# Kernel optimization log

Measured on AMD Instinct MI355X. Metric: run time of the kernel, lower is better.

Reference implementation:

```python
import jax, jax.numpy as jnp
import numpy as np

N, E, B = 50000, 600000, 64
ANN, D, STEPS, ETYPES, CLS = 64, 128, 5, 4, 10


def setup_inputs() -> dict:
    key = jax.random.key(0)
    ks = jax.random.split(key, 12)
    return {
        "annotation": jax.random.normal(ks[0], (N, ANN), jnp.float32),
        "src": jax.random.randint(ks[1], (E,), 0, N),
        "dst": jax.random.randint(ks[2], (E,), 0, N),
        "etypes": jax.random.randint(ks[3], (E,), 0, ETYPES),
        "node2graph": jnp.sort(jax.random.randint(ks[4], (N,), 0, B)),
        "labels": jax.random.randint(ks[5], (B,), 0, CLS),
        "W_lin": jax.random.normal(ks[6], (ETYPES, D, D), jnp.float32) / np.sqrt(D),
        "b_lin": jnp.zeros((ETYPES, D), jnp.float32),
        "W_ih": jax.random.normal(ks[7], (3 * D, D), jnp.float32) / np.sqrt(D),
        "W_hh": jax.random.normal(ks[8], (3 * D, D), jnp.float32) / np.sqrt(D),
        "b_ih": jnp.zeros((3 * D,), jnp.float32),
        "b_hh": jnp.zeros((3 * D,), jnp.float32),
        "gate_w": jax.random.normal(ks[9], (1, ANN + D), jnp.float32) / np.sqrt(ANN + D),
        "gate_b": jnp.zeros((1,), jnp.float32),
        "out_w": jax.random.normal(ks[10], (CLS, ANN + D), jnp.float32) / np.sqrt(ANN + D),
        "out_b": jnp.zeros((CLS,), jnp.float32),
    }


def reference(annotation, src, dst, etypes, node2graph, labels,
              W_lin, b_lin, W_ih, W_hh, b_ih, b_hh,
              gate_w, gate_b, out_w, out_b):
    n = annotation.shape[0]
    d = W_lin.shape[-1]
    nb = labels.shape[0]
    # h1 = [annotation | zeros]  -> [N, D]
    h = jnp.concatenate(
        [annotation, jnp.zeros((n, d - annotation.shape[1]), annotation.dtype)], -1)

    def step(hc, _):
        # per-edge-type linear transform of all nodes: [K, N, D]
        all_t = jnp.einsum('nd,kod->kno', hc, W_lin) + b_lin[:, None, :]
        m = all_t[etypes, src]                                  # [E, D] messages
        a = jax.ops.segment_sum(m, dst, num_segments=n)         # [N, D] aggregate
        # torch GRUCell: gates ordered (reset, update, new)
        gi = a @ W_ih.T + b_ih
        gh = hc @ W_hh.T + b_hh
        i_r, i_z, i_n = jnp.split(gi, 3, axis=-1)
        h_r, h_z, h_n = jnp.split(gh, 3, axis=-1)
        r = jax.nn.sigmoid(i_r + h_r)
        z = jax.nn.sigmoid(i_z + h_z)
        nt = jnp.tanh(i_n + r * h_n)
        return (1.0 - z) * nt + z * hc, None

    h, _ = jax.lax.scan(step, h, None, length=STEPS)
    feat = jnp.concatenate([h, annotation], -1)                 # [N, D+ANN]
    # global attention pooling: segment softmax over nodes per graph
    gate = (feat @ gate_w.T + gate_b)[:, 0]                     # [N]
    gmax = jax.ops.segment_max(gate, node2graph, num_segments=nb)
    ex = jnp.exp(gate - gmax[node2graph])
    denom = jax.ops.segment_sum(ex, node2graph, num_segments=nb)
    alpha = ex / denom[node2graph]
    readout = jax.ops.segment_sum(feat * alpha[:, None], node2graph, num_segments=nb)
    logits = readout @ out_w.T + out_b                          # [B, CLS]
    preds = jnp.argmax(logits, -1)
    logp = jax.nn.log_softmax(logits, -1)
    loss = -jnp.mean(jnp.take_along_axis(logp, labels[:, None], axis=1))
    return loss, preds
```

## Files before the change

kernel.cpp:

```cpp
#include <hip/hip_runtime.h>
#include <math.h>

#define DD 128
#define ANND 64
#define NSTEPS 5
#define NTYPES 4
#define NCLS 10

typedef __attribute__((ext_vector_type(8))) short short8v;
typedef __attribute__((ext_vector_type(4))) float f32x4;

__device__ __forceinline__ void split2(float x, unsigned short& hi, unsigned short& lo) {
  unsigned u = __float_as_uint(x);
  unsigned hb = (u + 0x7FFFu + ((u >> 16) & 1u)) >> 16;
  hi = (unsigned short)hb;
  float r = x - __uint_as_float(hb << 16);
  unsigned v = __float_as_uint(r);
  lo = (unsigned short)((v + 0x7FFFu + ((v >> 16) & 1u)) >> 16);
}

__device__ __forceinline__ float bf2f(unsigned short u) {
  return __uint_as_float(((unsigned)u) << 16);
}
__device__ __forceinline__ float rec2(const unsigned short* hi, const unsigned short* lo, size_t i) {
  return bf2f(hi[i]) + bf2f(lo[i]);
}
__device__ __forceinline__ float lo16f(unsigned u) { return __uint_as_float(u << 16); }
__device__ __forceinline__ float hi16f(unsigned u) { return __uint_as_float(u & 0xffff0000u); }

__device__ __forceinline__ void gload16(const unsigned short* g, unsigned short* l) {
  __builtin_amdgcn_global_load_lds(
      (const __attribute__((address_space(1))) unsigned int*)(const void*)g,
      (__attribute__((address_space(3))) unsigned int*)(void*)l, 16, 0, 0);
}

__global__ void k_init(const float* __restrict__ ann,
    unsigned short* __restrict__ hhi, unsigned short* __restrict__ hlo, int n, int npad) {
  int idx = blockIdx.x * blockDim.x + threadIdx.x;
  if (idx >= npad * DD) return;
  int node = idx >> 7, d = idx & 127;
  float v = (node < n && d < ANND) ? ann[node * ANND + d] : 0.0f;
  unsigned short hi, lo; split2(v, hi, lo);
  hhi[idx] = hi; hlo[idx] = lo;
}

__global__ void k_deg4(const int* __restrict__ dst, const int* __restrict__ et,
    int* __restrict__ deg4, int e) {
  int i = blockIdx.x * blockDim.x + threadIdx.x;
  if (i < e) atomicAdd(&deg4[dst[i] * 4 + et[i]], 1);
}

__global__ __launch_bounds__(1024) void k_scan(const int* __restrict__ deg4,
    int* __restrict__ base, int n) {
  __shared__ int part[1024];
  int t = threadIdx.x;
  int chunk = (n + 1023) >> 10;
  int s = t * chunk, e = min(n, s + chunk);
  int sum = 0;
  for (int i = s; i < e; ++i) {
    const int4 d4 = *(const int4*)(deg4 + (size_t)i * 4);
    sum += d4.x + d4.y + d4.z + d4.w;
  }
  part[t] = sum;
  __syncthreads();
  int own = sum;
  for (int off = 1; off < 1024; off <<= 1) {
    int v = (t >= off) ? part[t - off] : 0;
    __syncthreads();
    part[t] += v;
    __syncthreads();
  }
  int run = part[t] - own;
  for (int i = s; i < e; ++i) {
    base[i] = run;
    const int4 d4 = *(const int4*)(deg4 + (size_t)i * 4);
    run += d4.x + d4.y + d4.z + d4.w;
  }
  if (s < n && e == n) base[n] = run;
}

__global__ void k_place(const int* __restrict__ src, const int* __restrict__ dst,
    const int* __restrict__ et, const int* __restrict__ base, int* __restrict__ cursor,
    int* __restrict__ cpack, int e) {
  int i = blockIdx.x * blockDim.x + threadIdx.x;
  if (i >= e) return;
  int d = dst[i];
  int pos = base[d] + atomicAdd(&cursor[d], 1);
  cpack[pos] = src[i] | (et[i] << 18);
}

__global__ void k_aggh(const unsigned* __restrict__ hhiU, const unsigned* __restrict__ hloU,
    const int* __restrict__ base, const int* __restrict__ cpack,
    unsigned* __restrict__ A3hiU, unsigned* __restrict__ A3loU, int nbase, int cc) {
  int w = threadIdx.x >> 6;
  int lane = threadIdx.x & 63;
  int local = blockIdx.x * 4 + w;
  if (local >= cc) return;
  int node = nbase + local;
  int s = base[node], e = base[node + 1];
  float a0x = 0.f, a0y = 0.f, a1x = 0.f, a1y = 0.f;
  float a2x = 0.f, a2y = 0.f, a3x = 0.f, a3y = 0.f;
  for (int t0 = s; t0 < e; t0 += 64) {
    int cnt = min(64, e - t0);
    int mypk = (t0 + lane < e) ? cpack[t0 + lane] : 0;
    int i = 0;
    for (; i + 4 <= cnt; i += 4) {
      int pk0 = __shfl(mypk, i), pk1 = __shfl(mypk, i + 1);
      int pk2 = __shfl(mypk, i + 2), pk3 = __shfl(mypk, i + 3);
      unsigned uh0 = hhiU[(size_t)(pk0 & 0x3ffff) * 64 + lane];
      unsigned ul0 = hloU[(size_t)(pk0 & 0x3ffff) * 64 + lane];
      unsigned uh1 = hhiU[(size_t)(pk1 & 0x3ffff) * 64 + lane];
      unsigned ul1 = hloU[(size_t)(pk1 & 0x3ffff) * 64 + lane];
      unsigned uh2 = hhiU[(size_t)(pk2 & 0x3ffff) * 64 + lane];
      unsigned ul2 = hloU[(size_t)(pk2 & 0x3ffff) * 64 + lane];
      unsigned uh3 = hhiU[(size_t)(pk3 & 0x3ffff) * 64 + lane];
      unsigned ul3 = hloU[(size_t)(pk3 & 0x3ffff) * 64 + lane];
      float v0x = lo16f(uh0) + lo16f(ul0), v0y = hi16f(uh0) + hi16f(ul0);
      float v1x = lo16f(uh1) + lo16f(ul1), v1y = hi16f(uh1) + hi16f(ul1);
      float v2x = lo16f(uh2) + lo16f(ul2), v2y = hi16f(uh2) + hi16f(ul2);
      float v3x = lo16f(uh3) + lo16f(ul3), v3y = hi16f(uh3) + hi16f(ul3);
      int t;
      t = pk0 >> 18;
      if (t == 0) { a0x += v0x; a0y += v0y; } else if (t == 1) { a1x += v0x; a1y += v0y; }
      else if (t == 2) { a2x += v0x; a2y += v0y; } else { a3x += v0x; a3y += v0y; }
      t = pk1 >> 18;
      if (t == 0) { a0x += v1x; a0y += v1y; } else if (t == 1) { a1x += v1x; a1y += v1y; }
      else if (t == 2) { a2x += v1x; a2y += v1y; } else { a3x += v1x; a3y += v1y; }
      t = pk2 >> 18;
      if (t == 0) { a0x += v2x; a0y += v2y; } else if (t == 1) { a1x += v2x; a1y += v2y; }
      else if (t == 2) { a2x += v2x; a2y += v2y; } else { a3x += v2x; a3y += v2y; }
      t = pk3 >> 18;
      if (t == 0) { a0x += v3x; a0y += v3y; } else if (t == 1) { a1x += v3x; a1y += v3y; }
      else if (t == 2) { a2x += v3x; a2y += v3y; } else { a3x += v3x; a3y += v3y; }
    }
    for (; i < cnt; ++i) {
      int pk = __shfl(mypk, i);
      unsigned uh = hhiU[(size_t)(pk & 0x3ffff) * 64 + lane];
      unsigned ul = hloU[(size_t)(pk & 0x3ffff) * 64 + lane];
      float vx = lo16f(uh) + lo16f(ul), vy = hi16f(uh) + hi16f(ul);
      int t = pk >> 18;
      if (t == 0) { a0x += vx; a0y += vy; } else if (t == 1) { a1x += vx; a1y += vy; }
      else if (t == 2) { a2x += vx; a2y += vy; } else { a3x += vx; a3y += vy; }
    }
  }
  size_t bu = (size_t)local * 256 + lane;
  unsigned short h0, l0, h1, l1;
  split2(a0x, h0, l0); split2(a0y, h1, l1);
  A3hiU[bu] = (unsigned)h0 | ((unsigned)h1 << 16);
  A3loU[bu] = (unsigned)l0 | ((unsigned)l1 << 16);
  split2(a1x, h0, l0); split2(a1y, h1, l1);
  A3hiU[bu + 64] = (unsigned)h0 | ((unsigned)h1 << 16);
  A3loU[bu + 64] = (unsigned)l0 | ((unsigned)l1 << 16);
  split2(a2x, h0, l0); split2(a2y, h1, l1);
  A3hiU[bu + 128] = (unsigned)h0 | ((unsigned)h1 << 16);
  A3loU[bu + 128] = (unsigned)l0 | ((unsigned)l1 << 16);
  split2(a3x, h0, l0); split2(a3y, h1, l1);
  A3hiU[bu + 192] = (unsigned)h0 | ((unsigned)h1 << 16);
  A3loU[bu + 192] = (unsigned)l0 | ((unsigned)l1 << 16);
}

__global__ void k_fusew(const float* __restrict__ Wih, const float* __restrict__ Wlin,
    float* __restrict__ VW) {
  int idx = blockIdx.x * blockDim.x + threadIdx.x;
  if (idx >= 384 * 512) return;
  int c = idx >> 9, kd = idx & 511;
  int k = kd >> 7, d = kd & 127;
  const float* wi = Wih + (size_t)c * DD;
  const float* wl = Wlin + (size_t)k * DD * DD + d;
  float s = 0.f;
  for (int o = 0; o < DD; ++o) s += wi[o] * wl[(size_t)o * DD];
  VW[idx] = s;
}

__global__ void k_wbig(const float* __restrict__ VW, const float* __restrict__ Whh,
    unsigned short* __restrict__ WbH, unsigned short* __restrict__ WbL) {
  int idx = blockIdx.x * blockDim.x + threadIdx.x;
  if (idx >= 512 * 640) return;
  int c = idx / 640, k = idx % 640;
  float v;
  if (c < 256)      v = (k < 512) ? VW[(size_t)c * 512 + k] : Whh[(size_t)c * DD + (k - 512)];
  else if (c < 384) v = (k < 512) ? VW[(size_t)c * 512 + k] : 0.f;
  else              v = (k < 512) ? 0.f : Whh[(size_t)(c - 128) * DD + (k - 512)];
  int g = c >> 7, d = c & 127;
  int cn = ((d >> 5) << 7) + (((d >> 4) & 1) << 6) + (g << 4) + (d & 15);
  unsigned short h, l; split2(v, h, l);
  WbH[(size_t)cn * 640 + k] = h;
  WbL[(size_t)cn * 640 + k] = l;
}

__global__ void k_fuseb(const float* __restrict__ Wih, const float* __restrict__ bih,
    const float* __restrict__ bhh, const float* __restrict__ blin,
    float* __restrict__ bias_big, float* __restrict__ cb4) {
  int c = blockIdx.x * blockDim.x + threadIdx.x;
  if (c >= 512) return;
  float b;
  if (c < 256) b = bih[c] + bhh[c];
  else if (c < 384) b = bih[c];
  else b = bhh[c - 128];
  bias_big[c] = b;
  for (int k = 0; k < NTYPES; ++k) {
    float s = 0.f;
    if (c < 384) {
      const float* wi = Wih + (size_t)c * DD;
      const float* bl = blin + (size_t)k * DD;
      for (int o = 0; o < DD; ++o) s += wi[o] * bl[o];
    }
    cb4[k * 512 + c] = s;
  }
}

__global__ __launch_bounds__(256) void k_gru8(
    const unsigned short* __restrict__ A3hi, const unsigned short* __restrict__ A3lo,
    const unsigned short* __restrict__ Hhi, const unsigned short* __restrict__ Hlo,
    const unsigned short* __restrict__ WbH, const unsigned short* __restrict__ WbL,
    const float* __restrict__ bias_big, const float* __restrict__ cb4,
    const int* __restrict__ deg4,
    unsigned short* __restrict__ Ohi, unsigned short* __restrict__ Olo,
    int nbase, int cc) {
  __shared__ unsigned short ldsX[4096];
  __shared__ unsigned short ldsW[12288];
  int tid = threadIdx.x;
  int wc = tid >> 6, lane = tid & 63;
  int lr = lane & 15, lk = lane >> 4;
  int rowbase = blockIdx.y * 64;
  int ytile = blockIdx.x;
  int wtb = ytile * 256;
  f32x4 acc[4][4];
  #pragma unroll
  for (int mm = 0; mm < 4; ++mm)
    #pragma unroll
    for (int g = 0; g < 4; ++g) acc[mm][g] = (f32x4){0.f, 0.f, 0.f, 0.f};

  int srow = tid >> 2, sc0 = tid & 3;
  int xcs = sc0 ^ ((srow >> 1) & 3);
  int wwb = (tid & ~63) * 8;

  for (int it = 0; it < 20; ++it) {
    int k0 = it * 32;
    __syncthreads();
    {
      const unsigned short *xsH, *xsL;
      if (k0 < 512) {
        size_t off = (size_t)(rowbase + srow) * 512 + k0 + xcs * 8;
        xsH = A3hi + off; xsL = A3lo + off;
      } else {
        size_t off = (size_t)(nbase + rowbase + srow) * DD + (k0 - 512) + xcs * 8;
        xsH = Hhi + off; xsL = Hlo + off;
      }
      gload16(xsH, ldsX + wwb);
      gload16(xsL, ldsX + 2048 + wwb);
    }
    int skip = (k0 < 512) ? 3 : 2;
    #pragma unroll
    for (int i2 = 0; i2 < 3; ++i2) {
      int rc = i2 * 64 + srow;
      int grp = rc / 48, rem = rc - grp * 48;
      int s = rem >> 4, w16 = rem & 15;
      int g = s + (s >= skip ? 1 : 0);
      int srcrow = grp * 64 + g * 16 + w16;
      int wcs = sc0 ^ ((rc >> 1) & 3);
      size_t woff = (size_t)(wtb + srcrow) * 640 + k0 + wcs * 8;
      unsigned short* wdst = ldsW + i2 * 2048 + wwb;
      gload16(WbH + woff, wdst);
      gload16(WbL + woff, wdst + 6144);
    }
    __syncthreads();

    int nnSkip = skip;
    short8v xh[4], xl[4];
    #pragma unroll
    for (int mm = 0; mm < 4; ++mm) {
      int r = mm * 16 + lr;
      int a = r * 32 + ((lk ^ ((r >> 1) & 3)) << 3);
      xh[mm] = *(const short8v*)(ldsX + a);
      xl[mm] = *(const short8v*)(ldsX + 2048 + a);
    }
    #pragma unroll
    for (int nn = 0; nn < 4; ++nn) {
      if (nn == nnSkip) continue;
      int s = nn - (nn > nnSkip ? 1 : 0);
      int rc = wc * 48 + s * 16 + lr;
      int a = rc * 32 + ((lk ^ ((rc >> 1) & 3)) << 3);
      short8v wh = *(const short8v*)(ldsW + a);
      short8v wl = *(const short8v*)(ldsW + 6144 + a);
      #pragma unroll
      for (int mm = 0; mm < 4; ++mm) {
        acc[mm][nn] = __builtin_amdgcn_mfma_f32_16x16x32_bf16(xh[mm], wh, acc[mm][nn], 0, 0, 0);
        acc[mm][nn] = __builtin_amdgcn_mfma_f32_16x16x32_bf16(xh[mm], wl, acc[mm][nn], 0, 0, 0);
        acc[mm][nn] = __builtin_amdgcn_mfma_f32_16x16x32_bf16(xl[mm], wh, acc[mm][nn], 0, 0, 0);
      }
    }
  }

  int d = ytile * 64 + wc * 16 + lr;
  float bsr = bias_big[d], bsz = bias_big[128 + d];
  float bgn = bias_big[256 + d], bhn = bias_big[384 + d];
  float cbr[4], cbz[4], cbn[4];
  #pragma unroll
  for (int k = 0; k < 4; ++k) {
    cbr[k] = cb4[k * 512 + d];
    cbz[k] = cb4[k * 512 + 128 + d];
    cbn[k] = cb4[k * 512 + 256 + d];
  }
  #pragma unroll
  for (int mm = 0; mm < 4; ++mm) {
    #pragma unroll
    for (int j = 0; j < 4; ++j) {
      int row = rowbase + mm * 16 + lk * 4 + j;
      if (row < cc) {
        int4 dg = *(const int4*)(deg4 + (size_t)row * 4);
        float s_r = acc[mm][0][j] + bsr + dg.x * cbr[0] + dg.y * cbr[1] + dg.z * cbr[2] + dg.w * cbr[3];
        float s_z = acc[mm][1][j] + bsz + dg.x * cbz[0] + dg.y * cbz[1] + dg.z * cbz[2] + dg.w * cbz[3];
        float g_n = acc[mm][2][j] + bgn + dg.x * cbn[0] + dg.y * cbn[1] + dg.z * cbn[2] + dg.w * cbn[3];
        float h_n = acc[mm][3][j] + bhn;
        float r = 1.f / (1.f + expf(-s_r));
        float z = 1.f / (1.f + expf(-s_z));
        float nt = tanhf(g_n + r * h_n);
        size_t gidx = (size_t)(nbase + row) * DD + d;
        float hv = (1.f - z) * nt + z * rec2(Hhi, Hlo, gidx);
        unsigned short uh, ul; split2(hv, uh, ul);
        Ohi[gidx] = uh; Olo[gidx] = ul;
      }
    }
  }
}

__global__ void k_gate(const unsigned short* __restrict__ hhi,
    const unsigned short* __restrict__ hlo, const float* __restrict__ ann,
    const float* __restrict__ gw, const float* __restrict__ gb,
    float* __restrict__ gate, int n) {
  int gt = blockIdx.x * blockDim.x + threadIdx.x;
  int wv = gt >> 6;
  int lane = threadIdx.x & 63;
  if (wv >= n) return;
  float p = rec2(hhi, hlo, (size_t)wv * DD + lane) * gw[lane]
          + rec2(hhi, hlo, (size_t)wv * DD + 64 + lane) * gw[64 + lane]
          + ann[(size_t)wv * ANND + lane] * gw[128 + lane];
  for (int off = 32; off; off >>= 1) p += __shfl_down(p, off);
  if (lane == 0) gate[wv] = p + gb[0];
}

__global__ void k_bounds(const int* __restrict__ n2g, int* __restrict__ startg,
    int* __restrict__ endg, int n) {
  int i = blockIdx.x * blockDim.x + threadIdx.x;
  if (i >= n) return;
  int g = n2g[i];
  if (i == 0 || n2g[i - 1] != g) startg[g] = i;
  if (i == n - 1 || n2g[i + 1] != g) endg[g] = i + 1;
}

__global__ __launch_bounds__(256) void k_mden(const float* __restrict__ gate,
    const int* __restrict__ startg, const int* __restrict__ endg,
    float* __restrict__ mg, float* __restrict__ invg) {
  __shared__ float red[256];
  int g = blockIdx.x;
  int s = startg[g], e = endg[g];
  int tid = threadIdx.x;
  float m = -1e30f;
  for (int i = s + tid; i < e; i += 256) m = fmaxf(m, gate[i]);
  red[tid] = m; __syncthreads();
  for (int off = 128; off; off >>= 1) {
    if (tid < off) red[tid] = fmaxf(red[tid], red[tid + off]);
    __syncthreads();
  }
  m = red[0];
  __syncthreads();
  float sum = 0.f;
  for (int i = s + tid; i < e; i += 256) sum += expf(gate[i] - m);
  red[tid] = sum; __syncthreads();
  for (int off = 128; off; off >>= 1) {
    if (tid < off) red[tid] += red[tid + off];
    __syncthreads();
  }
  if (tid == 0) { mg[g] = m; invg[g] = (s < e) ? 1.f / red[0] : 0.f; }
}

__global__ __launch_bounds__(256) void k_pool2(const float* __restrict__ gate,
    const unsigned* __restrict__ hhiU, const unsigned* __restrict__ hloU,
    const float* __restrict__ ann, const int* __restrict__ startg,
    const int* __restrict__ endg, const float* __restrict__ mg,
    const float* __restrict__ invg, float* __restrict__ readout) {
  __shared__ float redx[256], redy[256];
  int g = blockIdx.x;
  int s = startg[g], e = endg[g];
  int nl = threadIdx.x >> 6, lane = threadIdx.x & 63;
  float m = mg[g], inv = invg[g];
  if (blockIdx.y == 0) {
    float ax = 0.f, ay = 0.f;
    for (int i = s + nl; i < e; i += 4) {
      float al = expf(gate[i] - m) * inv;
      unsigned uh = hhiU[(size_t)i * 64 + lane];
      unsigned ul = hloU[(size_t)i * 64 + lane];
      ax += al * (lo16f(uh) + lo16f(ul));
      ay += al * (hi16f(uh) + hi16f(ul));
    }
    redx[threadIdx.x] = ax; redy[threadIdx.x] = ay;
    __syncthreads();
    if (nl == 0) {
      float sx = redx[lane] + redx[64 + lane] + redx[128 + lane] + redx[192 + lane];
      float sy = redy[lane] + redy[64 + lane] + redy[128 + lane] + redy[192 + lane];
      readout[g * (DD + ANND) + 2 * lane] = sx;
      readout[g * (DD + ANND) + 2 * lane + 1] = sy;
    }
  } else {
    float acc = 0.f;
    for (int i = s + nl; i < e; i += 4) {
      float al = expf(gate[i] - m) * inv;
      acc += al * ann[(size_t)i * ANND + lane];
    }
    redx[threadIdx.x] = acc;
    __syncthreads();
    if (nl == 0)
      readout[g * (DD + ANND) + DD + lane] =
          redx[lane] + redx[64 + lane] + redx[128 + lane] + redx[192 + lane];
  }
}

__global__ void k_logits(const float* __restrict__ readout, const float* __restrict__ ow,
    const float* __restrict__ ob, const int* __restrict__ labels,
    float* __restrict__ out, int B) {
  __shared__ float lsum[64];
  int g = threadIdx.x;
  float loss_c = 0.f;
  if (g < B) {
    float lg[NCLS];
    float mx = -1e30f;
    int best = 0;
    for (int c = 0; c < NCLS; ++c) {
      float acc = ob[c];
      const float* r = readout + g * (DD + ANND);
      const float* w = ow + c * (DD + ANND);
      for (int d = 0; d < DD + ANND; ++d) acc += r[d] * w[d];
      lg[c] = acc;
      if (acc > mx) { mx = acc; best = c; }
    }
    float se = 0.f;
    for (int c = 0; c < NCLS; ++c) se += expf(lg[c] - mx);
    float lse = mx + logf(se);
    loss_c = -(lg[labels[g]] - lse);
    out[1 + g] = (float)best;
  }
  lsum[threadIdx.x] = loss_c;
  __syncthreads();
  for (int off = 32; off; off >>= 1) {
    if (threadIdx.x < off) lsum[threadIdx.x] += lsum[threadIdx.x + off];
    __syncthreads();
  }
  if (threadIdx.x == 0) out[0] = lsum[0] / (float)B;
}

extern "C" void kernel_launch(void* const* d_in, const int* in_sizes, int n_in,
                              void* d_out, int out_size, void* d_ws, size_t ws_size,
                              hipStream_t stream) {
  const float* annotation = (const float*)d_in[0];
  const int*   src        = (const int*)d_in[1];
  const int*   dst        = (const int*)d_in[2];
  const int*   et         = (const int*)d_in[3];
  const int*   n2g        = (const int*)d_in[4];
  const int*   labels     = (const int*)d_in[5];
  const float* W_lin      = (const float*)d_in[6];
  const float* b_lin      = (const float*)d_in[7];
  const float* W_ih       = (const float*)d_in[8];
  const float* W_hh       = (const float*)d_in[9];
  const float* b_ih       = (const float*)d_in[10];
  const float* b_hh       = (const float*)d_in[11];
  const float* gate_w     = (const float*)d_in[12];
  const float* gate_b     = (const float*)d_in[13];
  const float* out_w      = (const float*)d_in[14];
  const float* out_b      = (const float*)d_in[15];

  int N = in_sizes[0] / ANND;
  int E = in_sizes[1];
  int B = in_sizes[5];
  int Np = (N + 127) & ~127;

  auto rup = [](size_t b) { return (b + 255) & ~(size_t)255; };
  size_t fixed = 0;
  fixed += 4 * rup((size_t)Np * DD * 2);
  fixed += rup((size_t)N * 4);
  fixed += rup((size_t)B * (DD + ANND) * 4);
  fixed += 4 * rup((size_t)B * 4);
  fixed += rup((size_t)(N + 1) * 4);
  fixed += rup((size_t)N * 4);
  fixed += rup((size_t)N * 16);
  fixed += rup((size_t)E * 4);
  fixed += rup(384 * 512 * 4);
  fixed += 2 * rup(512 * 640 * 2);
  fixed += rup(512 * 4) + rup(4 * 512 * 4);
  size_t slack = 1 << 20;
  size_t avail = (ws_size > fixed + slack) ? ws_size - fixed - slack : 0;
  long long ch = (long long)(avail / 2048);
  int CH = (int)((ch / 128) * 128);
  if (CH < 128) CH = 128;
  if (CH > Np) CH = Np;

  char* wsP = (char*)d_ws;
  auto alloc = [&](size_t bytes) -> void* {
    void* p = (void*)wsP;
    wsP += (bytes + 255) & ~(size_t)255;
    return p;
  };
  unsigned short* hP_hi[2], *hP_lo[2];
  hP_hi[0] = (unsigned short*)alloc((size_t)Np * DD * 2);
  hP_lo[0] = (unsigned short*)alloc((size_t)Np * DD * 2);
  hP_hi[1] = (unsigned short*)alloc((size_t)Np * DD * 2);
  hP_lo[1] = (unsigned short*)alloc((size_t)Np * DD * 2);
  float* gate = (float*)alloc((size_t)N * 4);
  float* readout = (float*)alloc((size_t)B * (DD + ANND) * 4);
  int* startg = (int*)alloc((size_t)B * 4);
  int* endg   = (int*)alloc((size_t)B * 4);
  float* mg   = (float*)alloc((size_t)B * 4);
  float* invg = (float*)alloc((size_t)B * 4);
  int* base   = (int*)alloc((size_t)(N + 1) * 4);
  int* cursor = (int*)alloc((size_t)N * 4);
  int* deg4   = (int*)alloc((size_t)N * 16);
  int* cpack  = (int*)alloc((size_t)E * 4);
  float* VW   = (float*)alloc(384 * 512 * 4);
  unsigned short* WbH = (unsigned short*)alloc(512 * 640 * 2);
  unsigned short* WbL = (unsigned short*)alloc(512 * 640 * 2);
  float* bias_big = (float*)alloc(512 * 4);
  float* cb4  = (float*)alloc(4 * 512 * 4);
  unsigned short* A3hi = (unsigned short*)alloc((size_t)CH * 512 * 2);
  unsigned short* A3lo = (unsigned short*)alloc((size_t)CH * 512 * 2);

  k_init<<<(Np * DD + 255) / 256, 256, 0, stream>>>(annotation, hP_hi[0], hP_lo[0], N, Np);
  hipMemsetAsync(cursor, 0, (size_t)N * 4, stream);
  hipMemsetAsync(deg4, 0, (size_t)N * 16, stream);
  hipMemsetAsync(startg, 0x7f, (size_t)B * 4, stream);
  hipMemsetAsync(endg, 0, (size_t)B * 4, stream);
  k_deg4<<<(E + 255) / 256, 256, 0, stream>>>(dst, et, deg4, E);
  k_scan<<<1, 1024, 0, stream>>>(deg4, base, N);
  k_place<<<(E + 255) / 256, 256, 0, stream>>>(src, dst, et, base, cursor, cpack, E);
  k_bounds<<<(N + 255) / 256, 256, 0, stream>>>(n2g, startg, endg, N);
  k_fusew<<<(384 * 512 + 255) / 256, 256, 0, stream>>>(W_ih, W_lin, VW);
  k_wbig<<<(512 * 640 + 255) / 256, 256, 0, stream>>>(VW, W_hh, WbH, WbL);
  k_fuseb<<<2, 256, 0, stream>>>(W_ih, b_ih, b_hh, b_lin, bias_big, cb4);

  int cur = 0;
  for (int s = 0; s < NSTEPS; ++s) {
    int nxt = cur ^ 1;
    for (int nbase = 0; nbase < N; nbase += CH) {
      int cc = min(CH, N - nbase);
      int cgrid = (cc + 63) / 64;
      k_aggh<<<(cc + 3) / 4, 256, 0, stream>>>(
          (const unsigned*)hP_hi[cur], (const unsigned*)hP_lo[cur], base, cpack,
          (unsigned*)A3hi, (unsigned*)A3lo, nbase, cc);
      k_gru8<<<dim3(2, cgrid), 256, 0, stream>>>(A3hi, A3lo,
          hP_hi[cur], hP_lo[cur], WbH, WbL, bias_big, cb4,
          deg4 + (size_t)nbase * 4, hP_hi[nxt], hP_lo[nxt], nbase, cc);
    }
    cur ^= 1;
  }

  k_gate<<<(N * 64 + 255) / 256, 256, 0, stream>>>(
      hP_hi[cur], hP_lo[cur], annotation, gate_w, gate_b, gate, N);
  k_mden<<<B, 256, 0, stream>>>(gate, startg, endg, mg, invg);
  k_pool2<<<dim3(B, 2), 256, 0, stream>>>(gate, (const unsigned*)hP_hi[cur],
      (const unsigned*)hP_lo[cur], annotation, startg, endg, mg, invg, readout);
  k_logits<<<1, 64, 0, stream>>>(readout, out_w, out_b, labels, (float*)d_out, B);
}
```

Before: 1.165 ms.

## Interleave hidden-state hi/lo halves per node row for single contiguous gathers

Stores the split-bf16 hidden state as one array where each node row holds 128 hi values followed by 128 lo values, so each neighbour gather reads one contiguous 512-byte row. Previously it issued two separate 256-byte loads from distinct hi and lo arrays. In the aggregation kernel, lanes 0-31 accumulate hi parts and lanes 32-63 lo parts, combined with a cross-half shuffle before writing. The edge loop is also unrolled to 8 loads in flight. The GRU, gate and pooling kernels are updated to the new indexing; half the lanes now idle during the final split-and-store.

Result: no change. 1.178 ms (+1.1%).

```diff
diff --git a/kernel.cpp b/kernel.cpp
--- a/kernel.cpp
+++ b/kernel.cpp
@@ -22,9 +22,6 @@
 __device__ __forceinline__ float bf2f(unsigned short u) {
   return __uint_as_float(((unsigned)u) << 16);
 }
-__device__ __forceinline__ float rec2(const unsigned short* hi, const unsigned short* lo, size_t i) {
-  return bf2f(hi[i]) + bf2f(lo[i]);
-}
 __device__ __forceinline__ float lo16f(unsigned u) { return __uint_as_float(u << 16); }
 __device__ __forceinline__ float hi16f(unsigned u) { return __uint_as_float(u & 0xffff0000u); }
 
@@ -35,13 +32,14 @@
 }
 
 __global__ void k_init(const float* __restrict__ ann,
-    unsigned short* __restrict__ hhi, unsigned short* __restrict__ hlo, int n, int npad) {
+    unsigned short* __restrict__ hI, int n, int npad) {
   int idx = blockIdx.x * blockDim.x + threadIdx.x;
   if (idx >= npad * DD) return;
   int node = idx >> 7, d = idx & 127;
   float v = (node < n && d < ANND) ? ann[node * ANND + d] : 0.0f;
   unsigned short hi, lo; split2(v, hi, lo);
-  hhi[idx] = hi; hlo[idx] = lo;
+  hI[(size_t)node * 256 + d] = hi;
+  hI[(size_t)node * 256 + 128 + d] = lo;
 }
 
 __global__ void k_deg4(const int* __restrict__ dst, const int* __restrict__ et,
@@ -89,74 +87,74 @@
   cpack[pos] = src[i] | (et[i] << 18);
 }
 
-__global__ void k_aggh(const unsigned* __restrict__ hhiU, const unsigned* __restrict__ hloU,
-    const int* __restrict__ base, const int* __restrict__ cpack,
-    unsigned* __restrict__ A3hiU, unsigned* __restrict__ A3loU, int nbase, int cc) {
+__global__ void k_aggh(const uint2* __restrict__ hI2, const int* __restrict__ base,
+    const int* __restrict__ cpack, unsigned short* __restrict__ A3hi,
+    unsigned short* __restrict__ A3lo, int nbase, int cc) {
   int w = threadIdx.x >> 6;
   int lane = threadIdx.x & 63;
   int local = blockIdx.x * 4 + w;
   if (local >= cc) return;
   int node = nbase + local;
   int s = base[node], e = base[node + 1];
-  float a0x = 0.f, a0y = 0.f, a1x = 0.f, a1y = 0.f;
-  float a2x = 0.f, a2y = 0.f, a3x = 0.f, a3y = 0.f;
+  float4 a0 = make_float4(0.f,0.f,0.f,0.f), a1 = a0, a2 = a0, a3 = a0;
   for (int t0 = s; t0 < e; t0 += 64) {
     int cnt = min(64, e - t0);
     int mypk = (t0 + lane < e) ? cpack[t0 + lane] : 0;
     int i = 0;
-    for (; i + 4 <= cnt; i += 4) {
-      int pk0 = __shfl(mypk, i), pk1 = __shfl(mypk, i + 1);
-      int pk2 = __shfl(mypk, i + 2), pk3 = __shfl(mypk, i + 3);
-      unsigned uh0 = hhiU[(size_t)(pk0 & 0x3ffff) * 64 + lane];
-      unsigned ul0 = hloU[(size_t)(pk0 & 0x3ffff) * 64 + lane];
-      unsigned uh1 = hhiU[(size_t)(pk1 & 0x3ffff) * 64 + lane];
-      unsigned ul1 = hloU[(size_t)(pk1 & 0x3ffff) * 64 + lane];
-      unsigned uh2 = hhiU[(size_t)(pk2 & 0x3ffff) * 64 + lane];
-      unsigned ul2 = hloU[(size_t)(pk2 & 0x3ffff) * 64 + lane];
-      unsigned uh3 = hhiU[(size_t)(pk3 & 0x3ffff) * 64 + lane];
-      unsigned ul3 = hloU[(size_t)(pk3 & 0x3ffff) * 64 + lane];
-      float v0x = lo16f(uh0) + lo16f(ul0), v0y = hi16f(uh0) + hi16f(ul0);
-      float v1x = lo16f(uh1) + lo16f(ul1), v1y = hi16f(uh1) + hi16f(ul1);
-      float v2x = lo16f(uh2) + lo16f(ul2), v2y = hi16f(uh2) + hi16f(ul2);
-      float v3x = lo16f(uh3) + lo16f(ul3), v3y = hi16f(uh3) + hi16f(ul3);
-      int t;
-      t = pk0 >> 18;
-      if (t == 0) { a0x += v0x; a0y += v0y; } else if (t == 1) { a1x += v0x; a1y += v0y; }
-      else if (t == 2) { a2x += v0x; a2y += v0y; } else { a3x += v0x; a3y += v0y; }
-      t = pk1 >> 18;
-      if (t == 0) { a0x += v1x; a0y += v1y; } else if (t == 1) { a1x += v1x; a1y += v1y; }
-      else if (t == 2) { a2x += v1x; a2y += v1y; } else { a3x += v1x; a3y += v1y; }
-      t = pk2 >> 18;
-      if (t == 0) { a0x += v2x; a0y += v2y; } else if (t == 1) { a1x += v2x; a1y += v2y; }
-      else if (t == 2) { a2x += v2x; a2y += v2y; } else { a3x += v2x; a3y += v2y; }
-      t = pk3 >> 18;
-      if (t == 0) { a0x += v3x; a0y += v3y; } else if (t == 1) { a1x += v3x; a1y += v3y; }
-      else if (t == 2) { a2x += v3x; a2y += v3y; } else { a3x += v3x; a3y += v3y; }
+    for (; i + 8 <= cnt; i += 8) {
+      int pk[8]; uint2 v[8];
+      #pragma unroll
+      for (int j = 0; j < 8; ++j) pk[j] = __shfl(mypk, i + j);
+      #pragma unroll
+      for (int j = 0; j < 8; ++j) v[j] = hI2[(size_t)(pk[j] & 0x3ffff) * 64 + lane];
+      #pragma unroll
+      for (int j = 0; j < 8; ++j) {
+        float f0 = lo16f(v[j].x), f1 = hi16f(v[j].x);
+        float f2 = lo16f(v[j].y), f3 = hi16f(v[j].y);
+        int t = pk[j] >> 18;
+        if (t == 0)      { a0.x += f0; a0.y += f1; a0.z += f2; a0.w += f3; }
+        else if (t == 1) { a1.x += f0; a1.y += f1; a1.z += f2; a1.w += f3; }
+        else if (t == 2) { a2.x += f0; a2.y += f1; a2.z += f2; a2.w += f3; }
+        else             { a3.x += f0; a3.y += f1; a3.z += f2; a3.w += f3; }
+      }
     }
     for (; i < cnt; ++i) {
       int pk = __shfl(mypk, i);
-      unsigned uh = hhiU[(size_t)(pk & 0x3ffff) * 64 + lane];
-      unsigned ul = hloU[(size_t)(pk & 0x3ffff) * 64 + lane];
-      float vx = lo16f(uh) + lo16f(ul), vy = hi16f(uh) + hi16f(ul);
+      uint2 vv = hI2[(size_t)(pk & 0x3ffff) * 64 + lane];
+      float f0 = lo16f(vv.x), f1 = hi16f(vv.x), f2 = lo16f(vv.y), f3 = hi16f(vv.y);
       int t = pk >> 18;
-      if (t == 0) { a0x += vx; a0y += vy; } else if (t == 1) { a1x += vx; a1y += vy; }
-      else if (t == 2) { a2x += vx; a2y += vy; } else { a3x += vx; a3y += vy; }
-    }
-  }
-  size_t bu = (size_t)local * 256 + lane;
-  unsigned short h0, l0, h1, l1;
-  split2(a0x, h0, l0); split2(a0y, h1, l1);
-  A3hiU[bu] = (unsigned)h0 | ((unsigned)h1 << 16);
-  A3loU[bu] = (unsigned)l0 | ((unsigned)l1 << 16);
-  split2(a1x, h0, l0); split2(a1y, h1, l1);
-  A3hiU[bu + 64] = (unsigned)h0 | ((unsigned)h1 << 16);
-  A3loU[bu + 64] = (unsigned)l0 | ((unsigned)l1 << 16);
-  split2(a2x, h0, l0); split2(a2y, h1, l1);
-  A3hiU[bu + 128] = (unsigned)h0 | ((unsigned)h1 << 16);
-  A3loU[bu + 128] = (unsigned)l0 | ((unsigned)l1 << 16);
-  split2(a3x, h0, l0); split2(a3y, h1, l1);
-  A3hiU[bu + 192] = (unsigned)h0 | ((unsigned)h1 << 16);
-  A3loU[bu + 192] = (unsigned)l0 | ((unsigned)l1 << 16);
+      if (t == 0)      { a0.x += f0; a0.y += f1; a0.z += f2; a0.w += f3; }
+      else if (t == 1) { a1.x += f0; a1.y += f1; a1.z += f2; a1.w += f3; }
+      else if (t == 2) { a2.x += f0; a2.y += f1; a2.z += f2; a2.w += f3; }
+      else             { a3.x += f0; a3.y += f1; a3.z += f2; a3.w += f3; }
+    }
+  }
+  a0.x += __shfl_down(a0.x, 32); a0.y += __shfl_down(a0.y, 32);
+  a0.z += __shfl_down(a0.z, 32); a0.w += __shfl_down(a0.w, 32);
+  a1.x += __shfl_down(a1.x, 32); a1.y += __shfl_down(a1.y, 32);
+  a1.z += __shfl_down(a1.z, 32); a1.w += __shfl_down(a1.w, 32);
+  a2.x += __shfl_down(a2.x, 32); a2.y += __shfl_down(a2.y, 32);
+  a2.z += __shfl_down(a2.z, 32); a2.w += __shfl_down(a2.w, 32);
+  a3.x += __shfl_down(a3.x, 32); a3.y += __shfl_down(a3.y, 32);
+  a3.z += __shfl_down(a3.z, 32); a3.w += __shfl_down(a3.w, 32);
+  if (lane < 32) {
+    ushort4* A3h4 = (ushort4*)A3hi;
+    ushort4* A3l4 = (ushort4*)A3lo;
+    size_t b4 = (size_t)local * 128 + lane;
+    ushort4 h4, l4;
+    split2(a0.x, h4.x, l4.x); split2(a0.y, h4.y, l4.y);
+    split2(a0.z, h4.z, l4.z); split2(a0.w, h4.w, l4.w);
+    A3h4[b4] = h4; A3l4[b4] = l4;
+    split2(a1.x, h4.x, l4.x); split2(a1.y, h4.y, l4.y);
+    split2(a1.z, h4.z, l4.z); split2(a1.w, h4.w, l4.w);
+    A3h4[b4 + 32] = h4; A3l4[b4 + 32] = l4;
+    split2(a2.x, h4.x, l4.x); split2(a2.y, h4.y, l4.y);
+    split2(a2.z, h4.z, l4.z); split2(a2.w, h4.w, l4.w);
+    A3h4[b4 + 64] = h4; A3l4[b4 + 64] = l4;
+    split2(a3.x, h4.x, l4.x); split2(a3.y, h4.y, l4.y);
+    split2(a3.z, h4.z, l4.z); split2(a3.w, h4.w, l4.w);
+    A3h4[b4 + 96] = h4; A3l4[b4 + 96] = l4;
+  }
 }
 
 __global__ void k_fusew(const float* __restrict__ Wih, const float* __restrict__ Wlin,
@@ -211,12 +209,10 @@
 
 __global__ __launch_bounds__(256) void k_gru8(
     const unsigned short* __restrict__ A3hi, const unsigned short* __restrict__ A3lo,
-    const unsigned short* __restrict__ Hhi, const unsigned short* __restrict__ Hlo,
-    const unsigned short* __restrict__ WbH, const unsigned short* __restrict__ WbL,
-    const float* __restrict__ bias_big, const float* __restrict__ cb4,
-    const int* __restrict__ deg4,
-    unsigned short* __restrict__ Ohi, unsigned short* __restrict__ Olo,
-    int nbase, int cc) {
+    const unsigned short* __restrict__ HI, const unsigned short* __restrict__ WbH,
+    const unsigned short* __restrict__ WbL, const float* __restrict__ bias_big,
+    const float* __restrict__ cb4, const int* __restrict__ deg4,
+    unsigned short* __restrict__ OI, int nbase, int cc) {
   __shared__ unsigned short ldsX[4096];
   __shared__ unsigned short ldsW[12288];
   int tid = threadIdx.x;
@@ -244,8 +240,8 @@
         size_t off = (size_t)(rowbase + srow) * 512 + k0 + xcs * 8;
         xsH = A3hi + off; xsL = A3lo + off;
       } else {
-        size_t off = (size_t)(nbase + rowbase + srow) * DD + (k0 - 512) + xcs * 8;
-        xsH = Hhi + off; xsL = Hlo + off;
+        size_t off = (size_t)(nbase + rowbase + srow) * 256 + (k0 - 512) + xcs * 8;
+        xsH = HI + off; xsL = HI + off + 128;
       }
       gload16(xsH, ldsX + wwb);
       gload16(xsL, ldsX + 2048 + wwb);
@@ -316,25 +312,27 @@
         float r = 1.f / (1.f + expf(-s_r));
         float z = 1.f / (1.f + expf(-s_z));
         float nt = tanhf(g_n + r * h_n);
-        size_t gidx = (size_t)(nbase + row) * DD + d;
-        float hv = (1.f - z) * nt + z * rec2(Hhi, Hlo, gidx);
+        size_t hb = (size_t)(nbase + row) * 256 + d;
+        float hold = bf2f(HI[hb]) + bf2f(HI[hb + 128]);
+        float hv = (1.f - z) * nt + z * hold;
         unsigned short uh, ul; split2(hv, uh, ul);
-        Ohi[gidx] = uh; Olo[gidx] = ul;
+        OI[hb] = uh; OI[hb + 128] = ul;
       }
     }
   }
 }
 
-__global__ void k_gate(const unsigned short* __restrict__ hhi,
-    const unsigned short* __restrict__ hlo, const float* __restrict__ ann,
+__global__ void k_gate(const unsigned short* __restrict__ hI, const float* __restrict__ ann,
     const float* __restrict__ gw, const float* __restrict__ gb,
     float* __restrict__ gate, int n) {
   int gt = blockIdx.x * blockDim.x + threadIdx.x;
   int wv = gt >> 6;
   int lane = threadIdx.x & 63;
   if (wv >= n) return;
-  float p = rec2(hhi, hlo, (size_t)wv * DD + lane) * gw[lane]
-          + rec2(hhi, hlo, (size_t)wv * DD + 64 + lane) * gw[64 + lane]
+  size_t b = (size_t)wv * 256;
+  float h0 = bf2f(hI[b + lane]) + bf2f(hI[b + 128 + lane]);
+  float h1 = bf2f(hI[b + 64 + lane]) + bf2f(hI[b + 192 + lane]);
+  float p = h0 * gw[lane] + h1 * gw[64 + lane]
           + ann[(size_t)wv * ANND + lane] * gw[128 + lane];
   for (int off = 32; off; off >>= 1) p += __shfl_down(p, off);
   if (lane == 0) gate[wv] = p + gb[0];
@@ -376,10 +374,10 @@
 }
 
 __global__ __launch_bounds__(256) void k_pool2(const float* __restrict__ gate,
-    const unsigned* __restrict__ hhiU, const unsigned* __restrict__ hloU,
-    const float* __restrict__ ann, const int* __restrict__ startg,
-    const int* __restrict__ endg, const float* __restrict__ mg,
-    const float* __restrict__ invg, float* __restrict__ readout) {
+    const unsigned* __restrict__ hIU, const float* __restrict__ ann,
+    const int* __restrict__ startg, const int* __restrict__ endg,
+    const float* __restrict__ mg, const float* __restrict__ invg,
+    float* __restrict__ readout) {
   __shared__ float redx[256], redy[256];
   int g = blockIdx.x;
   int s = startg[g], e = endg[g];
@@ -389,8 +387,8 @@
     float ax = 0.f, ay = 0.f;
     for (int i = s + nl; i < e; i += 4) {
       float al = expf(gate[i] - m) * inv;
-      unsigned uh = hhiU[(size_t)i * 64 + lane];
-      unsigned ul = hloU[(size_t)i * 64 + lane];
+      unsigned uh = hIU[(size_t)i * 128 + lane];
+      unsigned ul = hIU[(size_t)i * 128 + 64 + lane];
       ax += al * (lo16f(uh) + lo16f(ul));
       ay += al * (hi16f(uh) + hi16f(ul));
     }
@@ -476,7 +474,7 @@
 
   auto rup = [](size_t b) { return (b + 255) & ~(size_t)255; };
   size_t fixed = 0;
-  fixed += 4 * rup((size_t)Np * DD * 2);
+  fixed += 2 * rup((size_t)Np * 512);
   fixed += rup((size_t)N * 4);
   fixed += rup((size_t)B * (DD + ANND) * 4);
   fixed += 4 * rup((size_t)B * 4);
@@ -500,11 +498,9 @@
     wsP += (bytes + 255) & ~(size_t)255;
     return p;
   };
-  unsigned short* hP_hi[2], *hP_lo[2];
-  hP_hi[0] = (unsigned short*)alloc((size_t)Np * DD * 2);
-  hP_lo[0] = (unsigned short*)alloc((size_t)Np * DD * 2);
-  hP_hi[1] = (unsigned short*)alloc((size_t)Np * DD * 2);
-  hP_lo[1] = (unsigned short*)alloc((size_t)Np * DD * 2);
+  unsigned short* hP[2];
+  hP[0] = (unsigned short*)alloc((size_t)Np * 512);
+  hP[1] = (unsigned short*)alloc((size_t)Np * 512);
   float* gate = (float*)alloc((size_t)N * 4);
   float* readout = (float*)alloc((size_t)B * (DD + ANND) * 4);
   int* startg = (int*)alloc((size_t)B * 4);
@@ -523,7 +519,7 @@
   unsigned short* A3hi = (unsigned short*)alloc((size_t)CH * 512 * 2);
   unsigned short* A3lo = (unsigned short*)alloc((size_t)CH * 512 * 2);
 
-  k_init<<<(Np * DD + 255) / 256, 256, 0, stream>>>(annotation, hP_hi[0], hP_lo[0], N, Np);
+  k_init<<<(Np * DD + 255) / 256, 256, 0, stream>>>(annotation, hP[0], N, Np);
   hipMemsetAsync(cursor, 0, (size_t)N * 4, stream);
   hipMemsetAsync(deg4, 0, (size_t)N * 16, stream);
   hipMemsetAsync(startg, 0x7f, (size_t)B * 4, stream);
@@ -543,19 +539,18 @@
       int cc = min(CH, N - nbase);
       int cgrid = (cc + 63) / 64;
       k_aggh<<<(cc + 3) / 4, 256, 0, stream>>>(
-          (const unsigned*)hP_hi[cur], (const unsigned*)hP_lo[cur], base, cpack,
-          (unsigned*)A3hi, (unsigned*)A3lo, nbase, cc);
+          (const uint2*)hP[cur], base, cpack, A3hi, A3lo, nbase, cc);
       k_gru8<<<dim3(2, cgrid), 256, 0, stream>>>(A3hi, A3lo,
-          hP_hi[cur], hP_lo[cur], WbH, WbL, bias_big, cb4,
-          deg4 + (size_t)nbase * 4, hP_hi[nxt], hP_lo[nxt], nbase, cc);
+          hP[cur], WbH, WbL, bias_big, cb4,
+          deg4 + (size_t)nbase * 4, hP[nxt], nbase, cc);
     }
     cur ^= 1;
   }
 
   k_gate<<<(N * 64 + 255) / 256, 256, 0, stream>>>(
-      hP_hi[cur], hP_lo[cur], annotation, gate_w, gate_b, gate, N);
+      hP[cur], annotation, gate_w, gate_b, gate, N);
   k_mden<<<B, 256, 0, stream>>>(gate, startg, endg, mg, invg);
-  k_pool2<<<dim3(B, 2), 256, 0, stream>>>(gate, (const unsigned*)hP_hi[cur],
-      (const unsigned*)hP_lo[cur], annotation, startg, endg, mg, invg, readout);
+  k_pool2<<<dim3(B, 2), 256, 0, stream>>>(gate, (const unsigned*)hP[cur],
+      annotation, startg, endg, mg, invg, readout);
   k_logits<<<1, 64, 0, stream>>>(readout, out_w, out_b, labels, (float*)d_out, B);
 }
```
